# Kernel tuning notes

Measured on AMD Instinct MI355X. Metric: run time of the kernel, lower is better.

Reference implementation:

```python
import jax, jax.numpy as jnp
import numpy as np

D_MODEL = 1024
NUM_HEADS = 16
HEAD_DIM = D_MODEL // NUM_HEADS


def setup_inputs() -> dict:
    key = jax.random.key(0)
    k_x, k_wqkv, k_bqkv, k_wo, k_bo = jax.random.split(key, 5)
    x = jax.random.normal(k_x, (2, 2048, D_MODEL), dtype=jnp.float32)
    s = 1.0 / np.sqrt(D_MODEL)
    W_qkv = jax.random.uniform(k_wqkv, (D_MODEL, 3 * D_MODEL), jnp.float32, -s, s)
    b_qkv = jax.random.uniform(k_bqkv, (3 * D_MODEL,), jnp.float32, -s, s)
    W_o = jax.random.uniform(k_wo, (D_MODEL, D_MODEL), jnp.float32, -s, s)
    b_o = jax.random.uniform(k_bo, (D_MODEL,), jnp.float32, -s, s)
    return {"x": x, "W_qkv": W_qkv, "b_qkv": b_qkv, "W_o": W_o, "b_o": b_o}


def reference(x, W_qkv, b_qkv, W_o, b_o):
    B, S, D = x.shape
    # fused QKV projection: [B,S,3D]
    qkv = jnp.einsum('bsd,de->bse', x, W_qkv) + b_qkv
    # [B,S,H,3*hd] -> [B,H,S,3*hd]
    qkv = qkv.reshape(B, S, NUM_HEADS, 3 * HEAD_DIM).transpose(0, 2, 1, 3)
    q, k, v = jnp.split(qkv, 3, axis=-1)  # each [B,H,S,hd]
    scale = 1.0 / jnp.sqrt(jnp.asarray(HEAD_DIM, dtype=x.dtype))
    scores = jnp.einsum('bhqd,bhkd->bhqk', q, k) * scale  # [B,H,S,S]
    attn = jax.nn.softmax(scores, axis=-1)
    values = jnp.einsum('bhqk,bhkd->bhqd', attn, v)  # [B,H,S,hd]
    values = values.transpose(0, 2, 1, 3).reshape(B, S, D)
    out = jnp.einsum('bsd,de->bse', values, W_o) + b_o
    return out
```

## Files before the change

kernel.cpp:

```cpp
#include <hip/hip_runtime.h>
#include <stdint.h>
#include <stddef.h>

typedef _Float16 f16;
typedef _Float16 f16x8 __attribute__((ext_vector_type(8)));
typedef _Float16 f16x4 __attribute__((ext_vector_type(4)));
typedef float    f32x2 __attribute__((ext_vector_type(2)));
typedef float    f32x4 __attribute__((ext_vector_type(4)));
typedef float    f32x16 __attribute__((ext_vector_type(16)));
typedef int      i32x4 __attribute__((ext_vector_type(4)));
typedef int      i32x2 __attribute__((ext_vector_type(2)));

#define S_LEN 2048
#define DM    1024
#define NH    16
#define HD    64
#define NTOK  4096
#define NQKV  3072
#define QSCALE 0.18033688011112042f

#if __has_builtin(__builtin_amdgcn_exp2f)
#define EXP2(x) __builtin_amdgcn_exp2f(x)
#else
#define EXP2(x) __expf((x) * 0.69314718055994531f)
#endif

__device__ __forceinline__ void gl_lds16(const void* g, void* l) {
  __builtin_amdgcn_global_load_lds(
      (const __attribute__((address_space(1))) void*)g,
      (__attribute__((address_space(3))) void*)l, 16, 0, 0);
}

__device__ __forceinline__ void pl32_swap(int& a, int& b) {
#if __has_builtin(__builtin_amdgcn_permlane32_swap)
  i32x2 r = __builtin_amdgcn_permlane32_swap(a, b, false, false);
  a = r.x; b = r.y;
#else
  asm volatile("v_permlane32_swap_b32 %0, %1" : "+v"(a), "+v"(b));
#endif
}

__device__ __forceinline__ float swap_half(float x, int hi) {
  int a = __builtin_bit_cast(int, x);
  int b = a;
  pl32_swap(a, b);
  return __builtin_bit_cast(float, hi ? a : b);
}

__device__ __forceinline__ int pkrtz(float a, float b) {
  auto h = __builtin_amdgcn_cvt_pkrtz(a, b);
  return __builtin_bit_cast(int, h);
}

__device__ __forceinline__ f16x8 mk_frag(int a, int b, int c, int d) {
  i32x4 v = {a, b, c, d};
  return __builtin_bit_cast(f16x8, v);
}

__device__ __forceinline__ f32x2 pk2(const f32x16& v, int i) {
  f32x2 r = {v[2*i], v[2*i+1]};
  return r;
}

__global__ __launch_bounds__(256) void cvt_f16_kernel(const float* __restrict__ in,
                                                      f16* __restrict__ out, int n) {
  int i = (blockIdx.x * 256 + threadIdx.x) * 8;
  if (i >= n) return;
  float4 a = *(const float4*)(in + i);
  float4 b = *(const float4*)(in + i + 4);
  f16x8 v = {(f16)a.x,(f16)a.y,(f16)a.z,(f16)a.w,(f16)b.x,(f16)b.y,(f16)b.z,(f16)b.w};
  *(f16x8*)(out + i) = v;
}

__global__ __launch_bounds__(256) void cvt_tr_kernel(const float* __restrict__ in,
                                                     f16* __restrict__ out, int R, int C) {
  __shared__ float t[32][33];
  int c0 = blockIdx.x * 32, r0 = blockIdx.y * 32;
  int tx = threadIdx.x, ty = threadIdx.y;
  #pragma unroll
  for (int i = 0; i < 4; ++i)
    t[ty + i*8][tx] = in[(size_t)(r0 + ty + i*8) * C + c0 + tx];
  __syncthreads();
  #pragma unroll
  for (int i = 0; i < 4; ++i)
    out[(size_t)(c0 + ty + i*8) * R + r0 + tx] = (f16)t[tx][ty + i*8];
}

template<int EPI>
__global__ __launch_bounds__(256) void gemm128_kernel(
    const f16* __restrict__ A, const f16* __restrict__ Bt,
    const float* __restrict__ bias,
    f16* __restrict__ qb, f16* __restrict__ kb, f16* __restrict__ vtb,
    float* __restrict__ out)
{
  __shared__ f16 As[128*32];
  __shared__ f16 Bs[128*32];
  const int tid = threadIdx.x;
  const int wid = tid >> 6, lane = tid & 63;
  const int g = lane >> 4, r = lane & 15;
  const int flat = blockIdx.x;
  const int xcd = flat & 7, idx = flat >> 3;
  const int m0 = (xcd * 4 + (idx & 3)) * 128;
  const int n0 = (idx >> 2) * 128;
  const int wm = (wid >> 1) * 64, wn = (wid & 1) * 64;

  f32x4 acc[4][4] = {};
  const int srow = tid >> 2;
  const int sch  = tid & 3;

  for (int kt = 0; kt < DM/32; ++kt) {
    const int k0 = kt * 32;
    __syncthreads();
    #pragma unroll
    for (int c = 0; c < 2; ++c) {
      int row = c*64 + srow;
      int sw = (sch ^ ((row >> 1) & 3)) * 8;
      gl_lds16(A  + (size_t)(m0 + row) * DM + k0 + sw, (char*)As + c*4096 + tid*16);
      gl_lds16(Bt + (size_t)(n0 + row) * DM + k0 + sw, (char*)Bs + c*4096 + tid*16);
    }
    __syncthreads();
    f16x8 a[4], b[4];
    #pragma unroll
    for (int mt = 0; mt < 4; ++mt) {
      int rl = wm + mt*16 + r;
      a[mt] = *(const f16x8*)(As + rl*32 + ((g ^ ((rl >> 1) & 3)) * 8));
    }
    #pragma unroll
    for (int nt = 0; nt < 4; ++nt) {
      int cl = wn + nt*16 + r;
      b[nt] = *(const f16x8*)(Bs + cl*32 + ((g ^ ((cl >> 1) & 3)) * 8));
    }
    #pragma unroll
    for (int mt = 0; mt < 4; ++mt)
      #pragma unroll
      for (int nt = 0; nt < 4; ++nt)
        acc[mt][nt] = __builtin_amdgcn_mfma_f32_16x16x32_f16(a[mt], b[nt], acc[mt][nt], 0, 0, 0);
  }

  if (EPI == 0) {
    #pragma unroll
    for (int mt = 0; mt < 4; ++mt) {
      int row0 = m0 + wm + mt*16 + g*4;
      int b_ = row0 >> 11, s0 = row0 & 2047;
      #pragma unroll
      for (int nt = 0; nt < 4; ++nt) {
        int col = n0 + wn + nt*16 + r;
        float bv = bias[col];
        int h = col / 192;
        int cc = col - h*192;
        int which = cc >> 6, d = cc & 63;
        size_t bh = (size_t)(b_*NH + h);
        if (which == 2) {
          f16x4 v;
          #pragma unroll
          for (int i = 0; i < 4; ++i) v[i] = (f16)(acc[mt][nt][i] + bv);
          *(f16x4*)(vtb + (bh*HD + d)*S_LEN + s0) = v;
        } else if (which == 0) {
          #pragma unroll
          for (int i = 0; i < 4; ++i)
            qb[(bh*S_LEN + s0 + i)*HD + d] = (f16)((acc[mt][nt][i] + bv) * QSCALE);
        } else {
          #pragma unroll
          for (int i = 0; i < 4; ++i)
            kb[(bh*S_LEN + s0 + i)*HD + d] = (f16)(acc[mt][nt][i] + bv);
        }
      }
    }
  } else {
    #pragma unroll
    for (int mt = 0; mt < 4; ++mt) {
      int row0 = m0 + wm + mt*16 + g*4;
      #pragma unroll
      for (int nt = 0; nt < 4; ++nt) {
        int col = n0 + wn + nt*16 + r;
        float bv = bias[col];
        #pragma unroll
        for (int i = 0; i < 4; ++i)
          out[(size_t)(row0 + i)*DM + col] = acc[mt][nt][i] + bv;
      }
    }
  }
}

__global__ __launch_bounds__(512) void attn_kernel(
    const f16* __restrict__ qb, const f16* __restrict__ kb,
    const f16* __restrict__ vtb, f16* __restrict__ values)
{
  __shared__ __align__(16) char smem[66048];

  const int tid = threadIdx.x;
  const int wid = tid >> 6, lane = tid & 63;
  const int wq = wid & 3, wk = wid >> 2;
  const int ql = lane & 31, hi = lane >> 5;
  const int flat = blockIdx.x;
  const int xcd = flat & 7, idx = flat >> 3;
  const int bh = xcd * 4 + (idx & 3);
  const int q0 = (idx >> 2) * 128 + wq * 32;
  const f16* qh = qb  + (size_t)bh * S_LEN * HD;
  const f16* kh = kb  + (size_t)bh * S_LEN * HD;
  const f16* vh = vtb + (size_t)bh * HD * S_LEN;
  const int kbase0 = wk * 1024;
  const int htid = tid & 255;

  int koff[2], voff[2];
  #pragma unroll
  for (int c = 0; c < 2; ++c) {
    int ca = htid + c*256, pr = ca >> 4, pc = ca & 15, lc = pc ^ (pr & 15);
    int row2 = pr*2 + (lc >> 3), e8 = (lc & 7) * 8;
    koff[c] = row2 * HD + e8;
    voff[c] = row2 * S_LEN + e8;
  }

  f16x8 qf[4];
  #pragma unroll
  for (int dk = 0; dk < 4; ++dk)
    qf[dk] = *(const f16x8*)(qh + (size_t)(q0 + ql)*HD + dk*16 + hi*8);

  const int r0b = (ql >> 1) << 8;
  const int xv  = (ql >> 1) & 15;
  const int hb  = ((ql & 1) << 3) | hi;

  f32x2 lacc = {0.f, 0.f};
  f32x16 o0 = {}, o1 = {};
  f32x16 sX0, sX1, sY0, sY1;

  #define STAGE_K(kt_, buf_) do {                                          \
    const f16* ks_ = kh + (size_t)(kbase0 + (kt_)*64) * HD;                \
    char* kd_ = smem + (wk*2 + (buf_))*8192;                               \
    gl_lds16(ks_ + koff[0], kd_ + htid*16);                                \
    gl_lds16(ks_ + koff[1], kd_ + 4096 + htid*16);                         \
  } while (0)
  #define STAGE_V(kt_, buf_) do {                                          \
    const f16* vs_ = vh + (kbase0 + (kt_)*64);                             \
    char* vd_ = smem + 32768 + (wk*2 + (buf_))*8192;                       \
    gl_lds16(vs_ + voff[0], vd_ + htid*16);                                \
    gl_lds16(vs_ + voff[1], vd_ + 4096 + htid*16);                         \
  } while (0)

  #define QK_H(S_, KsC_, base_) do {                                       \
    S_ = (f32x16){};                                                       \
    _Pragma("unroll")                                                      \
    for (int dk = 0; dk < 4; ++dk) {                                       \
      int off = r0b + (((hb | (dk << 1)) ^ xv) << 4);                      \
      f16x8 kf = *(const f16x8*)((KsC_) + (base_) + off);                  \
      S_ = __builtin_amdgcn_mfma_f32_32x32x16_f16(kf, qf[dk], S_, 0, 0, 0);\
    }                                                                      \
  } while (0)

  #define EXP_H(S_, PFA_, PFB_) do {                                       \
    _Pragma("unroll")                                                      \
    for (int i = 0; i < 16; ++i) S_[i] = EXP2(S_[i]);                      \
    f32x2 sm[4];                                                           \
    _Pragma("unroll")                                                      \
    for (int i = 0; i < 4; ++i) sm[i] = pk2(S_, i) + pk2(S_, i + 4);       \
    sm[0] += sm[1]; sm[2] += sm[3]; lacc += sm[0] + sm[2];                 \
    int a = pkrtz(S_[0], S_[1]), b = pkrtz(S_[2], S_[3]);                  \
    int c = pkrtz(S_[4], S_[5]), d = pkrtz(S_[6], S_[7]);                  \
    pl32_swap(a, c); pl32_swap(b, d);                                      \
    PFA_ = mk_frag(a, b, c, d);                                            \
    a = pkrtz(S_[8],  S_[9]);  b = pkrtz(S_[10], S_[11]);                  \
    c = pkrtz(S_[12], S_[13]); d = pkrtz(S_[14], S_[15]);                  \
    pl32_swap(a, c); pl32_swap(b, d);                                      \
    PFB_ = mk_frag(a, b, c, d);                                            \
  } while (0)

  #define PVQ(VsC_) do {                                                   \
    __builtin_amdgcn_s_setprio(1);                                         \
    _Pragma("unroll")                                                      \
    for (int w = 0; w < 4; ++w) {                                          \
      int off = r0b + (((hb | (w << 1)) ^ xv) << 4);                       \
      f16x8 vf0 = *(const f16x8*)((VsC_) + off);                           \
      f16x8 vf1 = *(const f16x8*)((VsC_) + 4096 + off);                    \
      o0 = __builtin_amdgcn_mfma_f32_32x32x16_f16(pf[w], vf0, o0, 0, 0, 0);\
      o1 = __builtin_amdgcn_mfma_f32_32x32x16_f16(pf[w], vf1, o1, 0, 0, 0);\
    }                                                                      \
    __builtin_amdgcn_s_setprio(0);                                         \
  } while (0)

  #define BODY(SA0_, SA1_, SB0_, SB1_, kt_, cur_) do {                     \
    const char* KsN = smem + (wk*2 + ((cur_) ^ 1))*8192;                   \
    const char* VsC = smem + 32768 + (wk*2 + (cur_))*8192;                 \
    STAGE_V((kt_) + 1, (cur_) ^ 1);                                        \
    if ((kt_) < 14) STAGE_K((kt_) + 2, (cur_));                            \
    QK_H(SB0_, KsN, 0);                                                    \
    EXP_H(SA0_, pf[0], pf[1]);                                             \
    QK_H(SB1_, KsN, 4096);                                                 \
    EXP_H(SA1_, pf[2], pf[3]);                                             \
    PVQ(VsC);                                                              \
    __syncthreads();                                                       \
  } while (0)

  STAGE_K(0, 0); STAGE_V(0, 0); STAGE_K(1, 1);
  __syncthreads();
  f16x8 pf[4];
  {
    const char* Ks0 = smem + (wk*2)*8192;
    QK_H(sX0, Ks0, 0);
    QK_H(sX1, Ks0, 4096);
  }
  __syncthreads();

  for (int kt2 = 0; kt2 < 14; kt2 += 2) {
    BODY(sX0, sX1, sY0, sY1, kt2,     0);
    BODY(sY0, sY1, sX0, sX1, kt2 + 1, 1);
  }
  BODY(sX0, sX1, sY0, sY1, 14, 0);
  EXP_H(sY0, pf[0], pf[1]);
  EXP_H(sY1, pf[2], pf[3]);
  {
    const char* VsC = smem + 32768 + (wk*2 + 1)*8192;
    PVQ(VsC);
  }
  __syncthreads();

  #undef STAGE_K
  #undef STAGE_V
  #undef QK_H
  #undef EXP_H
  #undef PVQ
  #undef BODY

  float l_run = lacc.x + lacc.y;
  l_run += swap_half(l_run, hi);

  float* crow = ((float*)smem) + (wq*64 + lane)*36;
  float* cb   = (float*)(smem + 65536);
  if (wk == 1) {
    #pragma unroll
    for (int j = 0; j < 4; ++j) {
      f32x4 v0 = {o0[4*j], o0[4*j+1], o0[4*j+2], o0[4*j+3]};
      f32x4 v1 = {o1[4*j], o1[4*j+1], o1[4*j+2], o1[4*j+3]};
      *(f32x4*)(crow + j*4)      = v0;
      *(f32x4*)(crow + 16 + j*4) = v1;
    }
    crow[32] = l_run;
  }
  __syncthreads();
  if (wk == 0) {
    float inv = 1.0f / (l_run + crow[32]);
    cb[wq*32 + ql] = inv;
    f32x4 vinv[4], po0[4], po1[4];
    #pragma unroll
    for (int t = 0; t < 4; ++t) {
      vinv[t] = *(const f32x4*)&cb[wq*32 + hi*4 + t*8];
      po0[t]  = *(const f32x4*)(crow + t*4);
      po1[t]  = *(const f32x4*)(crow + 16 + t*4);
    }
    const int b_ = bh >> 4, h = bh & 15;
    #pragma unroll
    for (int t = 0; t < 4; ++t)
      #pragma unroll
      for (int i = 0; i < 4; ++i) {
        float v0 = (o0[t*4+i] + po0[t][i]) * vinv[t][i];
        float v1 = (o1[t*4+i] + po1[t][i]) * vinv[t][i];
        int qrow = q0 + 4*hi + 8*t + i;
        size_t base = (size_t)(b_*S_LEN + qrow) * DM + h*HD + ql;
        values[base]      = (f16)v0;
        values[base + 32] = (f16)v1;
      }
  }
}

extern "C" void kernel_launch(void* const* d_in, const int* in_sizes, int n_in,
                              void* d_out, int out_size, void* d_ws, size_t ws_size,
                              hipStream_t stream) {
  (void)in_sizes; (void)n_in; (void)out_size; (void)ws_size;
  const float* x    = (const float*)d_in[0];
  const float* Wqkv = (const float*)d_in[1];
  const float* bqkv = (const float*)d_in[2];
  const float* Wo   = (const float*)d_in[3];
  const float* bo   = (const float*)d_in[4];
  float* out = (float*)d_out;

  char* ws = (char*)d_ws;
  f16* x_h    = (f16*)(ws);
  f16* Wqkv_t = (f16*)(ws + ( 8ull<<20));
  f16* Wo_t   = (f16*)(ws + (14ull<<20));
  f16* qbuf   = (f16*)(ws + (16ull<<20));
  f16* kbuf   = (f16*)(ws + (24ull<<20));
  f16* vtbuf  = (f16*)(ws + (32ull<<20));
  f16* vals   = (f16*)(ws + (40ull<<20));

  cvt_f16_kernel<<<dim3(NTOK*DM/8/256), dim3(256), 0, stream>>>(x, x_h, NTOK*DM);
  cvt_tr_kernel<<<dim3(NQKV/32, DM/32), dim3(32, 8), 0, stream>>>(Wqkv, Wqkv_t, DM, NQKV);
  cvt_tr_kernel<<<dim3(DM/32, DM/32),  dim3(32, 8), 0, stream>>>(Wo, Wo_t, DM, DM);

  gemm128_kernel<0><<<dim3(768), dim3(256), 0, stream>>>(
      x_h, Wqkv_t, bqkv, qbuf, kbuf, vtbuf, nullptr);

  attn_kernel<<<dim3(512), dim3(512), 0, stream>>>(qbuf, kbuf, vtbuf, vals);

  gemm128_kernel<1><<<dim3(256), dim3(256), 0, stream>>>(
      vals, Wo_t, bo, nullptr, nullptr, nullptr, out);
}
```

Measured before the change: 117.4 us.

## Drop split-K attention waves and deepen GEMM K-tile to 64

The attention kernel no longer splits each 128-query block's key range across two wave groups. Each block now has 4 waves that walk all 2048 keys, which removes the LDS merge of partial outputs and denominators and halves LDS use, but doubles the serial loop length per wave. Separately, the GEMM kernel stages 64-wide K tiles with an 8-way XOR swizzle and issues two MFMA sub-steps per barrier pair, halving the number of syncs per output tile.

```diff
diff --git a/kernel.cpp b/kernel.cpp
--- a/kernel.cpp
+++ b/kernel.cpp
@@ -93,8 +93,8 @@
     f16* __restrict__ qb, f16* __restrict__ kb, f16* __restrict__ vtb,
     float* __restrict__ out)
 {
-  __shared__ f16 As[128*32];
-  __shared__ f16 Bs[128*32];
+  __shared__ f16 As[128*64];
+  __shared__ f16 Bs[128*64];
   const int tid = threadIdx.x;
   const int wid = tid >> 6, lane = tid & 63;
   const int g = lane >> 4, r = lane & 15;
@@ -105,36 +105,42 @@
   const int wm = (wid >> 1) * 64, wn = (wid & 1) * 64;
 
   f32x4 acc[4][4] = {};
-  const int srow = tid >> 2;
-  const int sch  = tid & 3;
-
-  for (int kt = 0; kt < DM/32; ++kt) {
-    const int k0 = kt * 32;
+  int soff[4];
+  #pragma unroll
+  for (int c = 0; c < 4; ++c) {
+    int ca = tid + c*256, pr = ca >> 3, pc = ca & 7, lc = pc ^ (pr & 7);
+    soff[c] = pr * DM + lc * 8;
+  }
+  const f16* Ab = A  + (size_t)m0 * DM;
+  const f16* Bb = Bt + (size_t)n0 * DM;
+
+  for (int kt = 0; kt < 16; ++kt) {
     __syncthreads();
     #pragma unroll
-    for (int c = 0; c < 2; ++c) {
-      int row = c*64 + srow;
-      int sw = (sch ^ ((row >> 1) & 3)) * 8;
-      gl_lds16(A  + (size_t)(m0 + row) * DM + k0 + sw, (char*)As + c*4096 + tid*16);
-      gl_lds16(Bt + (size_t)(n0 + row) * DM + k0 + sw, (char*)Bs + c*4096 + tid*16);
+    for (int c = 0; c < 4; ++c) {
+      gl_lds16(Ab + kt*64 + soff[c], (char*)As + c*4096 + tid*16);
+      gl_lds16(Bb + kt*64 + soff[c], (char*)Bs + c*4096 + tid*16);
     }
     __syncthreads();
-    f16x8 a[4], b[4];
-    #pragma unroll
-    for (int mt = 0; mt < 4; ++mt) {
-      int rl = wm + mt*16 + r;
-      a[mt] = *(const f16x8*)(As + rl*32 + ((g ^ ((rl >> 1) & 3)) * 8));
-    }
-    #pragma unroll
-    for (int nt = 0; nt < 4; ++nt) {
-      int cl = wn + nt*16 + r;
-      b[nt] = *(const f16x8*)(Bs + cl*32 + ((g ^ ((cl >> 1) & 3)) * 8));
-    }
-    #pragma unroll
-    for (int mt = 0; mt < 4; ++mt)
-      #pragma unroll
-      for (int nt = 0; nt < 4; ++nt)
-        acc[mt][nt] = __builtin_amdgcn_mfma_f32_16x16x32_f16(a[mt], b[nt], acc[mt][nt], 0, 0, 0);
+    #pragma unroll
+    for (int kk = 0; kk < 2; ++kk) {
+      f16x8 a[4], b[4];
+      #pragma unroll
+      for (int mt = 0; mt < 4; ++mt) {
+        int rl = wm + mt*16 + r;
+        a[mt] = *(const f16x8*)(As + rl*64 + (((kk*4 + g) ^ (rl & 7)) * 8));
+      }
+      #pragma unroll
+      for (int nt = 0; nt < 4; ++nt) {
+        int cl = wn + nt*16 + r;
+        b[nt] = *(const f16x8*)(Bs + cl*64 + (((kk*4 + g) ^ (cl & 7)) * 8));
+      }
+      #pragma unroll
+      for (int mt = 0; mt < 4; ++mt)
+        #pragma unroll
+        for (int nt = 0; nt < 4; ++nt)
+          acc[mt][nt] = __builtin_amdgcn_mfma_f32_16x16x32_f16(a[mt], b[nt], acc[mt][nt], 0, 0, 0);
+    }
   }
 
   if (EPI == 0) {
@@ -182,30 +188,27 @@
   }
 }
 
-__global__ __launch_bounds__(512) void attn_kernel(
+__global__ __launch_bounds__(256) void attn_kernel(
     const f16* __restrict__ qb, const f16* __restrict__ kb,
     const f16* __restrict__ vtb, f16* __restrict__ values)
 {
-  __shared__ __align__(16) char smem[66048];
+  __shared__ __align__(16) char smem[33280];
 
   const int tid = threadIdx.x;
   const int wid = tid >> 6, lane = tid & 63;
-  const int wq = wid & 3, wk = wid >> 2;
   const int ql = lane & 31, hi = lane >> 5;
   const int flat = blockIdx.x;
   const int xcd = flat & 7, idx = flat >> 3;
   const int bh = xcd * 4 + (idx & 3);
-  const int q0 = (idx >> 2) * 128 + wq * 32;
+  const int q0 = (idx >> 2) * 128 + wid * 32;
   const f16* qh = qb  + (size_t)bh * S_LEN * HD;
   const f16* kh = kb  + (size_t)bh * S_LEN * HD;
   const f16* vh = vtb + (size_t)bh * HD * S_LEN;
-  const int kbase0 = wk * 1024;
-  const int htid = tid & 255;
 
   int koff[2], voff[2];
   #pragma unroll
   for (int c = 0; c < 2; ++c) {
-    int ca = htid + c*256, pr = ca >> 4, pc = ca & 15, lc = pc ^ (pr & 15);
+    int ca = tid + c*256, pr = ca >> 4, pc = ca & 15, lc = pc ^ (pr & 15);
     int row2 = pr*2 + (lc >> 3), e8 = (lc & 7) * 8;
     koff[c] = row2 * HD + e8;
     voff[c] = row2 * S_LEN + e8;
@@ -225,16 +228,16 @@
   f32x16 sX0, sX1, sY0, sY1;
 
   #define STAGE_K(kt_, buf_) do {                                          \
-    const f16* ks_ = kh + (size_t)(kbase0 + (kt_)*64) * HD;                \
-    char* kd_ = smem + (wk*2 + (buf_))*8192;                               \
-    gl_lds16(ks_ + koff[0], kd_ + htid*16);                                \
-    gl_lds16(ks_ + koff[1], kd_ + 4096 + htid*16);                         \
+    const f16* ks_ = kh + (size_t)((kt_)*64) * HD;                         \
+    char* kd_ = smem + (buf_)*8192;                                        \
+    gl_lds16(ks_ + koff[0], kd_ + tid*16);                                 \
+    gl_lds16(ks_ + koff[1], kd_ + 4096 + tid*16);                          \
   } while (0)
   #define STAGE_V(kt_, buf_) do {                                          \
-    const f16* vs_ = vh + (kbase0 + (kt_)*64);                             \
-    char* vd_ = smem + 32768 + (wk*2 + (buf_))*8192;                       \
-    gl_lds16(vs_ + voff[0], vd_ + htid*16);                                \
-    gl_lds16(vs_ + voff[1], vd_ + 4096 + htid*16);                         \
+    const f16* vs_ = vh + (kt_)*64;                                        \
+    char* vd_ = smem + 16384 + (buf_)*8192;                                \
+    gl_lds16(vs_ + voff[0], vd_ + tid*16);                                 \
+    gl_lds16(vs_ + voff[1], vd_ + 4096 + tid*16);                          \
   } while (0)
 
   #define QK_H(S_, KsC_, base_) do {                                       \
@@ -264,13 +267,14 @@
     PFB_ = mk_frag(a, b, c, d);                                            \
   } while (0)
 
-  #define PVQ(VsC_) do {                                                   \
+  #define PVQ(buf_) do {                                                   \
+    const char* VsC = smem + 16384 + (buf_)*8192;                          \
     __builtin_amdgcn_s_setprio(1);                                         \
     _Pragma("unroll")                                                      \
     for (int w = 0; w < 4; ++w) {                                          \
       int off = r0b + (((hb | (w << 1)) ^ xv) << 4);                       \
-      f16x8 vf0 = *(const f16x8*)((VsC_) + off);                           \
-      f16x8 vf1 = *(const f16x8*)((VsC_) + 4096 + off);                    \
+      f16x8 vf0 = *(const f16x8*)(VsC + off);                              \
+      f16x8 vf1 = *(const f16x8*)(VsC + 4096 + off);                       \
       o0 = __builtin_amdgcn_mfma_f32_32x32x16_f16(pf[w], vf0, o0, 0, 0, 0);\
       o1 = __builtin_amdgcn_mfma_f32_32x32x16_f16(pf[w], vf1, o1, 0, 0, 0);\
     }                                                                      \
@@ -278,40 +282,32 @@
   } while (0)
 
   #define BODY(SA0_, SA1_, SB0_, SB1_, kt_, cur_) do {                     \
-    const char* KsN = smem + (wk*2 + ((cur_) ^ 1))*8192;                   \
-    const char* VsC = smem + 32768 + (wk*2 + (cur_))*8192;                 \
+    const char* KsN = smem + ((cur_) ^ 1)*8192;                            \
     STAGE_V((kt_) + 1, (cur_) ^ 1);                                        \
-    if ((kt_) < 14) STAGE_K((kt_) + 2, (cur_));                            \
+    if ((kt_) < 30) STAGE_K((kt_) + 2, (cur_));                            \
     QK_H(SB0_, KsN, 0);                                                    \
     EXP_H(SA0_, pf[0], pf[1]);                                             \
     QK_H(SB1_, KsN, 4096);                                                 \
     EXP_H(SA1_, pf[2], pf[3]);                                             \
-    PVQ(VsC);                                                              \
+    PVQ(cur_);                                                             \
     __syncthreads();                                                       \
   } while (0)
 
   STAGE_K(0, 0); STAGE_V(0, 0); STAGE_K(1, 1);
   __syncthreads();
   f16x8 pf[4];
-  {
-    const char* Ks0 = smem + (wk*2)*8192;
-    QK_H(sX0, Ks0, 0);
-    QK_H(sX1, Ks0, 4096);
-  }
+  QK_H(sX0, smem, 0);
+  QK_H(sX1, smem, 4096);
   __syncthreads();
 
-  for (int kt2 = 0; kt2 < 14; kt2 += 2) {
+  for (int kt2 = 0; kt2 < 30; kt2 += 2) {
     BODY(sX0, sX1, sY0, sY1, kt2,     0);
     BODY(sY0, sY1, sX0, sX1, kt2 + 1, 1);
   }
-  BODY(sX0, sX1, sY0, sY1, 14, 0);
+  BODY(sX0, sX1, sY0, sY1, 30, 0);
   EXP_H(sY0, pf[0], pf[1]);
   EXP_H(sY1, pf[2], pf[3]);
-  {
-    const char* VsC = smem + 32768 + (wk*2 + 1)*8192;
-    PVQ(VsC);
-  }
-  __syncthreads();
+  PVQ(1);
 
   #undef STAGE_K
   #undef STAGE_V
@@ -322,43 +318,25 @@
 
   float l_run = lacc.x + lacc.y;
   l_run += swap_half(l_run, hi);
-
-  float* crow = ((float*)smem) + (wq*64 + lane)*36;
-  float* cb   = (float*)(smem + 65536);
-  if (wk == 1) {
-    #pragma unroll
-    for (int j = 0; j < 4; ++j) {
-      f32x4 v0 = {o0[4*j], o0[4*j+1], o0[4*j+2], o0[4*j+3]};
-      f32x4 v1 = {o1[4*j], o1[4*j+1], o1[4*j+2], o1[4*j+3]};
-      *(f32x4*)(crow + j*4)      = v0;
-      *(f32x4*)(crow + 16 + j*4) = v1;
-    }
-    crow[32] = l_run;
-  }
+  float inv = 1.0f / l_run;
+  float* cb = (float*)(smem + 32768) + wid*32;
+  cb[ql] = inv;
   __syncthreads();
-  if (wk == 0) {
-    float inv = 1.0f / (l_run + crow[32]);
-    cb[wq*32 + ql] = inv;
-    f32x4 vinv[4], po0[4], po1[4];
-    #pragma unroll
-    for (int t = 0; t < 4; ++t) {
-      vinv[t] = *(const f32x4*)&cb[wq*32 + hi*4 + t*8];
-      po0[t]  = *(const f32x4*)(crow + t*4);
-      po1[t]  = *(const f32x4*)(crow + 16 + t*4);
-    }
-    const int b_ = bh >> 4, h = bh & 15;
-    #pragma unroll
-    for (int t = 0; t < 4; ++t)
-      #pragma unroll
-      for (int i = 0; i < 4; ++i) {
-        float v0 = (o0[t*4+i] + po0[t][i]) * vinv[t][i];
-        float v1 = (o1[t*4+i] + po1[t][i]) * vinv[t][i];
-        int qrow = q0 + 4*hi + 8*t + i;
-        size_t base = (size_t)(b_*S_LEN + qrow) * DM + h*HD + ql;
-        values[base]      = (f16)v0;
-        values[base + 32] = (f16)v1;
-      }
-  }
+  f32x4 vinv[4];
+  #pragma unroll
+  for (int t = 0; t < 4; ++t)
+    vinv[t] = *(const f32x4*)(cb + hi*4 + t*8);
+
+  const int b_ = bh >> 4, h = bh & 15;
+  #pragma unroll
+  for (int t = 0; t < 4; ++t)
+    #pragma unroll
+    for (int i = 0; i < 4; ++i) {
+      int qrow = q0 + 4*hi + 8*t + i;
+      size_t base = (size_t)(b_*S_LEN + qrow) * DM + h*HD + ql;
+      values[base]      = (f16)(o0[t*4+i] * vinv[t][i]);
+      values[base + 32] = (f16)(o1[t*4+i] * vinv[t][i]);
+    }
 }
 
 extern "C" void kernel_launch(void* const* d_in, const int* in_sizes, int n_in,
@@ -388,7 +366,7 @@
   gemm128_kernel<0><<<dim3(768), dim3(256), 0, stream>>>(
       x_h, Wqkv_t, bqkv, qbuf, kbuf, vtbuf, nullptr);
 
-  attn_kernel<<<dim3(512), dim3(512), 0, stream>>>(qbuf, kbuf, vtbuf, vals);
+  attn_kernel<<<dim3(512), dim3(256), 0, stream>>>(qbuf, kbuf, vtbuf, vals);
 
   gemm128_kernel<1><<<dim3(256), dim3(256), 0, stream>>>(
       vals, Wo_t, bo, nullptr, nullptr, nullptr, out);
```

After: 126.7 us. +7.9%, slower.

## Process 64 queries per warp to double K/V tile reuse in attention

Applied to the files above, without the earlier changes.

Each attention warp now handles two 32-query groups, so the block covers 256 query rows and the grid halves to 256 blocks. Every K/V fragment read from LDS feeds twice as many MFMAs. The software pipeline that overlapped QK of the next tile with exp/PV of the current tile is replaced by a simpler single-stage loop that stages K and V together. The cost is higher register pressure, fewer blocks than the 256 CUs can absorb well, and less overlap between MFMA and exp work.

```diff
diff --git a/kernel.cpp b/kernel.cpp
--- a/kernel.cpp
+++ b/kernel.cpp
@@ -186,7 +186,7 @@
     const f16* __restrict__ qb, const f16* __restrict__ kb,
     const f16* __restrict__ vtb, f16* __restrict__ values)
 {
-  __shared__ __align__(16) char smem[66048];
+  __shared__ __align__(16) char smem[67584];
 
   const int tid = threadIdx.x;
   const int wid = tid >> 6, lane = tid & 63;
@@ -195,7 +195,7 @@
   const int flat = blockIdx.x;
   const int xcd = flat & 7, idx = flat >> 3;
   const int bh = xcd * 4 + (idx & 3);
-  const int q0 = (idx >> 2) * 128 + wq * 32;
+  const int q0 = (idx >> 2) * 256 + wq * 64;
   const f16* qh = qb  + (size_t)bh * S_LEN * HD;
   const f16* kh = kb  + (size_t)bh * S_LEN * HD;
   const f16* vh = vtb + (size_t)bh * HD * S_LEN;
@@ -211,49 +211,63 @@
     voff[c] = row2 * S_LEN + e8;
   }
 
-  f16x8 qf[4];
+  f16x8 qfA[4], qfB[4];
   #pragma unroll
-  for (int dk = 0; dk < 4; ++dk)
-    qf[dk] = *(const f16x8*)(qh + (size_t)(q0 + ql)*HD + dk*16 + hi*8);
+  for (int dk = 0; dk < 4; ++dk) {
+    qfA[dk] = *(const f16x8*)(qh + (size_t)(q0 + ql)*HD + dk*16 + hi*8);
+    qfB[dk] = *(const f16x8*)(qh + (size_t)(q0 + 32 + ql)*HD + dk*16 + hi*8);
+  }
 
   const int r0b = (ql >> 1) << 8;
   const int xv  = (ql >> 1) & 15;
   const int hb  = ((ql & 1) << 3) | hi;
 
-  f32x2 lacc = {0.f, 0.f};
-  f32x16 o0 = {}, o1 = {};
-  f32x16 sX0, sX1, sY0, sY1;
-
-  #define STAGE_K(kt_, buf_) do {                                          \
+  f32x2 laccA = {0.f, 0.f}, laccB = {0.f, 0.f};
+  f32x16 oA0 = {}, oA1 = {}, oB0 = {}, oB1 = {};
+  f32x16 sA0, sA1, sB0, sB1;
+  const f32x16 ZERO = {};
+
+  #define STAGE(kt_, buf_) do {                                            \
     const f16* ks_ = kh + (size_t)(kbase0 + (kt_)*64) * HD;                \
+    const f16* vs_ = vh + (kbase0 + (kt_)*64);                             \
     char* kd_ = smem + (wk*2 + (buf_))*8192;                               \
+    char* vd_ = smem + 32768 + (wk*2 + (buf_))*8192;                       \
     gl_lds16(ks_ + koff[0], kd_ + htid*16);                                \
     gl_lds16(ks_ + koff[1], kd_ + 4096 + htid*16);                         \
-  } while (0)
-  #define STAGE_V(kt_, buf_) do {                                          \
-    const f16* vs_ = vh + (kbase0 + (kt_)*64);                             \
-    char* vd_ = smem + 32768 + (wk*2 + (buf_))*8192;                       \
     gl_lds16(vs_ + voff[0], vd_ + htid*16);                                \
     gl_lds16(vs_ + voff[1], vd_ + 4096 + htid*16);                         \
   } while (0)
 
-  #define QK_H(S_, KsC_, base_) do {                                       \
-    S_ = (f32x16){};                                                       \
+  #define QK_STEP(buf_) do {                                               \
+    const char* KsC = smem + (wk*2 + (buf_))*8192;                         \
+    {                                                                      \
+      int off0 = r0b + ((hb ^ xv) << 4);                                   \
+      f16x8 kf0 = *(const f16x8*)(KsC + off0);                             \
+      f16x8 kf1 = *(const f16x8*)(KsC + 4096 + off0);                      \
+      sA0 = __builtin_amdgcn_mfma_f32_32x32x16_f16(kf0, qfA[0], ZERO, 0, 0, 0); \
+      sB0 = __builtin_amdgcn_mfma_f32_32x32x16_f16(kf0, qfB[0], ZERO, 0, 0, 0); \
+      sA1 = __builtin_amdgcn_mfma_f32_32x32x16_f16(kf1, qfA[0], ZERO, 0, 0, 0); \
+      sB1 = __builtin_amdgcn_mfma_f32_32x32x16_f16(kf1, qfB[0], ZERO, 0, 0, 0); \
+    }                                                                      \
     _Pragma("unroll")                                                      \
-    for (int dk = 0; dk < 4; ++dk) {                                       \
+    for (int dk = 1; dk < 4; ++dk) {                                       \
       int off = r0b + (((hb | (dk << 1)) ^ xv) << 4);                      \
-      f16x8 kf = *(const f16x8*)((KsC_) + (base_) + off);                  \
-      S_ = __builtin_amdgcn_mfma_f32_32x32x16_f16(kf, qf[dk], S_, 0, 0, 0);\
+      f16x8 kf0 = *(const f16x8*)(KsC + off);                              \
+      f16x8 kf1 = *(const f16x8*)(KsC + 4096 + off);                       \
+      sA0 = __builtin_amdgcn_mfma_f32_32x32x16_f16(kf0, qfA[dk], sA0, 0, 0, 0); \
+      sB0 = __builtin_amdgcn_mfma_f32_32x32x16_f16(kf0, qfB[dk], sB0, 0, 0, 0); \
+      sA1 = __builtin_amdgcn_mfma_f32_32x32x16_f16(kf1, qfA[dk], sA1, 0, 0, 0); \
+      sB1 = __builtin_amdgcn_mfma_f32_32x32x16_f16(kf1, qfB[dk], sB1, 0, 0, 0); \
     }                                                                      \
   } while (0)
 
-  #define EXP_H(S_, PFA_, PFB_) do {                                       \
+  #define EXP_H(S_, LACC_, PFA_, PFB_) do {                                \
     _Pragma("unroll")                                                      \
     for (int i = 0; i < 16; ++i) S_[i] = EXP2(S_[i]);                      \
     f32x2 sm[4];                                                           \
     _Pragma("unroll")                                                      \
     for (int i = 0; i < 4; ++i) sm[i] = pk2(S_, i) + pk2(S_, i + 4);       \
-    sm[0] += sm[1]; sm[2] += sm[3]; lacc += sm[0] + sm[2];                 \
+    sm[0] += sm[1]; sm[2] += sm[3]; LACC_ += sm[0] + sm[2];                \
     int a = pkrtz(S_[0], S_[1]), b = pkrtz(S_[2], S_[3]);                  \
     int c = pkrtz(S_[4], S_[5]), d = pkrtz(S_[6], S_[7]);                  \
     pl32_swap(a, c); pl32_swap(b, d);                                      \
@@ -264,100 +278,87 @@
     PFB_ = mk_frag(a, b, c, d);                                            \
   } while (0)
 
-  #define PVQ(VsC_) do {                                                   \
+  #define PV_STEP(buf_) do {                                               \
+    const char* VsC = smem + 32768 + (wk*2 + (buf_))*8192;                 \
     __builtin_amdgcn_s_setprio(1);                                         \
     _Pragma("unroll")                                                      \
     for (int w = 0; w < 4; ++w) {                                          \
       int off = r0b + (((hb | (w << 1)) ^ xv) << 4);                       \
-      f16x8 vf0 = *(const f16x8*)((VsC_) + off);                           \
-      f16x8 vf1 = *(const f16x8*)((VsC_) + 4096 + off);                    \
-      o0 = __builtin_amdgcn_mfma_f32_32x32x16_f16(pf[w], vf0, o0, 0, 0, 0);\
-      o1 = __builtin_amdgcn_mfma_f32_32x32x16_f16(pf[w], vf1, o1, 0, 0, 0);\
+      f16x8 vf0 = *(const f16x8*)(VsC + off);                              \
+      f16x8 vf1 = *(const f16x8*)(VsC + 4096 + off);                       \
+      oA0 = __builtin_amdgcn_mfma_f32_32x32x16_f16(pfA[w], vf0, oA0, 0, 0, 0); \
+      oA1 = __builtin_amdgcn_mfma_f32_32x32x16_f16(pfA[w], vf1, oA1, 0, 0, 0); \
+      oB0 = __builtin_amdgcn_mfma_f32_32x32x16_f16(pfB[w], vf0, oB0, 0, 0, 0); \
+      oB1 = __builtin_amdgcn_mfma_f32_32x32x16_f16(pfB[w], vf1, oB1, 0, 0, 0); \
     }                                                                      \
     __builtin_amdgcn_s_setprio(0);                                         \
   } while (0)
 
-  #define BODY(SA0_, SA1_, SB0_, SB1_, kt_, cur_) do {                     \
-    const char* KsN = smem + (wk*2 + ((cur_) ^ 1))*8192;                   \
-    const char* VsC = smem + 32768 + (wk*2 + (cur_))*8192;                 \
-    STAGE_V((kt_) + 1, (cur_) ^ 1);                                        \
-    if ((kt_) < 14) STAGE_K((kt_) + 2, (cur_));                            \
-    QK_H(SB0_, KsN, 0);                                                    \
-    EXP_H(SA0_, pf[0], pf[1]);                                             \
-    QK_H(SB1_, KsN, 4096);                                                 \
-    EXP_H(SA1_, pf[2], pf[3]);                                             \
-    PVQ(VsC);                                                              \
-    __syncthreads();                                                       \
-  } while (0)
-
-  STAGE_K(0, 0); STAGE_V(0, 0); STAGE_K(1, 1);
+  f16x8 pfA[4], pfB[4];
+  STAGE(0, 0);
   __syncthreads();
-  f16x8 pf[4];
-  {
-    const char* Ks0 = smem + (wk*2)*8192;
-    QK_H(sX0, Ks0, 0);
-    QK_H(sX1, Ks0, 4096);
-  }
-  __syncthreads();
-
-  for (int kt2 = 0; kt2 < 14; kt2 += 2) {
-    BODY(sX0, sX1, sY0, sY1, kt2,     0);
-    BODY(sY0, sY1, sX0, sX1, kt2 + 1, 1);
-  }
-  BODY(sX0, sX1, sY0, sY1, 14, 0);
-  EXP_H(sY0, pf[0], pf[1]);
-  EXP_H(sY1, pf[2], pf[3]);
-  {
-    const char* VsC = smem + 32768 + (wk*2 + 1)*8192;
-    PVQ(VsC);
-  }
-  __syncthreads();
-
-  #undef STAGE_K
-  #undef STAGE_V
-  #undef QK_H
+
+  for (int kt = 0; kt < 16; ++kt) {
+    const int cur = kt & 1;
+    if (kt + 1 < 16) STAGE(kt + 1, cur ^ 1);
+    QK_STEP(cur);
+    EXP_H(sA0, laccA, pfA[0], pfA[1]);
+    EXP_H(sA1, laccA, pfA[2], pfA[3]);
+    EXP_H(sB0, laccB, pfB[0], pfB[1]);
+    EXP_H(sB1, laccB, pfB[2], pfB[3]);
+    PV_STEP(cur);
+    __syncthreads();
+  }
+  #undef STAGE
+  #undef QK_STEP
   #undef EXP_H
-  #undef PVQ
-  #undef BODY
-
-  float l_run = lacc.x + lacc.y;
-  l_run += swap_half(l_run, hi);
-
-  float* crow = ((float*)smem) + (wq*64 + lane)*36;
-  float* cb   = (float*)(smem + 65536);
+  #undef PV_STEP
+
+  float lA = laccA.x + laccA.y;  lA += swap_half(lA, hi);
+  float lB = laccB.x + laccB.y;  lB += swap_half(lB, hi);
+
+  const int slot = wq*64 + lane;
+  float* lpl = (float*)(smem + 65536);
+  float* ipl = (float*)(smem + 66560);
   if (wk == 1) {
     #pragma unroll
-    for (int j = 0; j < 4; ++j) {
-      f32x4 v0 = {o0[4*j], o0[4*j+1], o0[4*j+2], o0[4*j+3]};
-      f32x4 v1 = {o1[4*j], o1[4*j+1], o1[4*j+2], o1[4*j+3]};
-      *(f32x4*)(crow + j*4)      = v0;
-      *(f32x4*)(crow + 16 + j*4) = v1;
-    }
-    crow[32] = l_run;
+    for (int t = 0; t < 4; ++t) {
+      *(f32x4*)(smem + (0*8 + 0*4 + t)*4096 + slot*16) = (f32x4){oA0[4*t], oA0[4*t+1], oA0[4*t+2], oA0[4*t+3]};
+      *(f32x4*)(smem + (0*8 + 1*4 + t)*4096 + slot*16) = (f32x4){oA1[4*t], oA1[4*t+1], oA1[4*t+2], oA1[4*t+3]};
+      *(f32x4*)(smem + (1*8 + 0*4 + t)*4096 + slot*16) = (f32x4){oB0[4*t], oB0[4*t+1], oB0[4*t+2], oB0[4*t+3]};
+      *(f32x4*)(smem + (1*8 + 1*4 + t)*4096 + slot*16) = (f32x4){oB1[4*t], oB1[4*t+1], oB1[4*t+2], oB1[4*t+3]};
+    }
+    lpl[wq*64 + 0*32 + ql] = lA;
+    lpl[wq*64 + 1*32 + ql] = lB;
   }
   __syncthreads();
   if (wk == 0) {
-    float inv = 1.0f / (l_run + crow[32]);
-    cb[wq*32 + ql] = inv;
-    f32x4 vinv[4], po0[4], po1[4];
-    #pragma unroll
-    for (int t = 0; t < 4; ++t) {
-      vinv[t] = *(const f32x4*)&cb[wq*32 + hi*4 + t*8];
-      po0[t]  = *(const f32x4*)(crow + t*4);
-      po1[t]  = *(const f32x4*)(crow + 16 + t*4);
-    }
+    float invA = 1.0f / (lA + lpl[wq*64 + ql]);
+    float invB = 1.0f / (lB + lpl[wq*64 + 32 + ql]);
+    ipl[wq*64 + ql]      = invA;
+    ipl[wq*64 + 32 + ql] = invB;
+  }
+  __syncthreads();
+  if (wk == 0) {
     const int b_ = bh >> 4, h = bh & 15;
     #pragma unroll
-    for (int t = 0; t < 4; ++t)
+    for (int g2 = 0; g2 < 2; ++g2) {
+      const f32x16& s0 = g2 ? oB0 : oA0;
+      const f32x16& s1 = g2 ? oB1 : oA1;
       #pragma unroll
-      for (int i = 0; i < 4; ++i) {
-        float v0 = (o0[t*4+i] + po0[t][i]) * vinv[t][i];
-        float v1 = (o1[t*4+i] + po1[t][i]) * vinv[t][i];
-        int qrow = q0 + 4*hi + 8*t + i;
-        size_t base = (size_t)(b_*S_LEN + qrow) * DM + h*HD + ql;
-        values[base]      = (f16)v0;
-        values[base + 32] = (f16)v1;
+      for (int t = 0; t < 4; ++t) {
+        f32x4 p0 = *(const f32x4*)(smem + (g2*8 + 0*4 + t)*4096 + slot*16);
+        f32x4 p1 = *(const f32x4*)(smem + (g2*8 + 1*4 + t)*4096 + slot*16);
+        f32x4 iv = *(const f32x4*)(ipl + wq*64 + g2*32 + 4*hi + 8*t);
+        #pragma unroll
+        for (int i = 0; i < 4; ++i) {
+          int qrow = q0 + g2*32 + 4*hi + 8*t + i;
+          size_t base = (size_t)(b_*S_LEN + qrow) * DM + h*HD + ql;
+          values[base]      = (f16)((s0[4*t+i] + p0[i]) * iv[i]);
+          values[base + 32] = (f16)((s1[4*t+i] + p1[i]) * iv[i]);
+        }
       }
+    }
   }
 }
 
@@ -388,7 +389,7 @@
   gemm128_kernel<0><<<dim3(768), dim3(256), 0, stream>>>(
       x_h, Wqkv_t, bqkv, qbuf, kbuf, vtbuf, nullptr);
 
-  attn_kernel<<<dim3(512), dim3(512), 0, stream>>>(qbuf, kbuf, vtbuf, vals);
+  attn_kernel<<<dim3(256), dim3(512), 0, stream>>>(qbuf, kbuf, vtbuf, vals);
 
   gemm128_kernel<1><<<dim3(256), dim3(256), 0, stream>>>(
       vals, Wo_t, bo, nullptr, nullptr, nullptr, out);
```

Result: faster. 114.6 us (-2.4%).
